# Performance work log

Hardware: AMD Instinct MI355X
Metric: run time of the kernel (lower is better)

The kernel has to match this reference:

```python
import jax, jax.numpy as jnp
import numpy as np

K = 512
U = 2
TEMP_BERN = 0.67
TEMP_CAT = 0.67
EULER = 0.5772156649015329
EPS = 1e-8
UEPS = 1e-6


def setup_inputs() -> dict:
    key = jax.random.key(0)
    ks = jax.random.split(key, 3)
    B, D = 16384, 1024
    inputs = jax.random.normal(ks[0], (B, D), jnp.float32)
    # glorot-normal-ish init for mW
    mW = jax.random.normal(ks[1], (D, K * U), jnp.float32) * jnp.sqrt(2.0 / (D + K * U))
    sW = jnp.full((D, K * U), -5.0, jnp.float32)
    conc1 = jnp.full((K,), 2.0, jnp.float32)
    conc0 = jnp.full((K,), 0.5453, jnp.float32)
    t_pi = jax.random.uniform(ks[2], (D, K), jnp.float32, 4.0, 5.0)
    biases = jnp.full((K * U,), 0.1, jnp.float32)
    return {"inputs": inputs, "mW": mW, "sW": sW, "conc1": conc1,
            "conc0": conc0, "t_pi": t_pi, "biases": biases}


def _uniform(k, shape):
    return jax.random.uniform(k, shape, jnp.float32, UEPS, 1.0 - UEPS)


def reference(inputs, mW, sW, conc1, conc0, t_pi, biases):
    rk = jax.random.split(jax.random.key(42), 4)

    # --- reparameterized weights W = mW + eps * softplus(sW) ---
    sW_sp = jax.nn.softplus(sW)
    eps = jax.lax.stop_gradient(jax.random.normal(rk[0], mW.shape, jnp.float32))
    W = mW + eps * sW_sp
    kl_weights = -0.5 * jnp.mean(2.0 * sW_sp - jnp.square(mW) - jnp.square(sW_sp) + 1.0)
    layer_loss = kl_weights / 60000.0

    # --- IBP: relaxed Bernoulli sample of t_pi ([D, K]) ---
    u = _uniform(rk[1], t_pi.shape)
    logistic = jnp.log(u) - jnp.log1p(-u)
    z_sample = jax.nn.sigmoid((t_pi + logistic) / TEMP_BERN)  # bin_concrete_sample
    z = jnp.tile(z_sample, (1, U))  # [D, K*U], column order u*K+k (as in TF code)

    # Kumaraswamy stick-breaking prior: cumprod along axis 0 (TF default)
    a_sp = jax.nn.softplus(conc1)  # [K]
    b_sp = jax.nn.softplus(conc0)  # [K]
    uk = _uniform(rk[2], t_pi.shape)
    q_u = jnp.power(1.0 - jnp.power(uk, 1.0 / b_sp), 1.0 / a_sp)  # kumaraswamy_sample
    prior_pi = jnp.cumprod(q_u, axis=0)
    q = jax.nn.sigmoid(t_pi)
    kl_z = jnp.sum(q * (jnp.log(q + EPS) - jnp.log(prior_pi + EPS)))

    # KL(Kumaraswamy(a,b) || Beta(1,1)); (beta-1) series term vanishes
    kl_sticks = jnp.sum(((a_sp - 1.0) / a_sp) * (-EULER - jax.scipy.special.digamma(b_sp) - 1.0 / b_sp)
                        + jnp.log(a_sp * b_sp + EPS) - (b_sp - 1.0) / b_sp)
    layer_loss = layer_loss + kl_sticks + kl_z

    W = z * W
    out = inputs @ W + biases  # [B, K*U]

    # --- LWTA activation via Gumbel-softmax over U competitors ---
    logits = out.reshape(-1, K, U)  # [B, K, U]
    g = -jnp.log(-jnp.log(_uniform(rk[3], logits.shape)))
    xi = jax.nn.softmax((logits + g) / TEMP_CAT, axis=-1)  # concrete_sample
    out_act = (logits * xi).reshape(out.shape)
    q_xi = jax.nn.softmax(logits, axis=-1)
    kl_xi = jnp.mean(jnp.sum(q_xi * (jnp.log(q_xi + EPS) - jnp.log(1.0 / U)), axis=1))
    layer_loss = layer_loss + kl_xi

    return out_act, layer_loss
```

## Files before the change

### kernel.cpp

```cpp
#include <hip/hip_runtime.h>
#include <stdint.h>
#include <math.h>

#define B_N   16384
#define D_N   1024
#define K_N   512
#define KU_N  1024
#define EPS_F 1e-8f
#define TEMP  0.67f
#define EULERC 0.5772156649015329f

#define HEPS  524288
#define HU    262144
#define HG    8388608

typedef uint32_t u32;
typedef __attribute__((ext_vector_type(4))) float f32x4;
typedef __attribute__((ext_vector_type(4))) unsigned int u32x4;
typedef __attribute__((ext_vector_type(8))) __bf16 bf16x8;

#define TF_ROT(x, r) (((x) << (r)) | ((x) >> (32 - (r))))

__host__ __device__ static inline void threefry2x32(u32 k0, u32 k1,
                                                    u32 x0, u32 x1,
                                                    u32* o0, u32* o1) {
  u32 ks2 = k0 ^ k1 ^ 0x1BD11BDAu;
  x0 += k0; x1 += k1;
  x0 += x1; x1 = TF_ROT(x1, 13); x1 ^= x0;
  x0 += x1; x1 = TF_ROT(x1, 15); x1 ^= x0;
  x0 += x1; x1 = TF_ROT(x1, 26); x1 ^= x0;
  x0 += x1; x1 = TF_ROT(x1, 6);  x1 ^= x0;
  x0 += k1; x1 += ks2 + 1u;
  x0 += x1; x1 = TF_ROT(x1, 17); x1 ^= x0;
  x0 += x1; x1 = TF_ROT(x1, 29); x1 ^= x0;
  x0 += x1; x1 = TF_ROT(x1, 16); x1 ^= x0;
  x0 += x1; x1 = TF_ROT(x1, 24); x1 ^= x0;
  x0 += ks2; x1 += k0 + 2u;
  x0 += x1; x1 = TF_ROT(x1, 13); x1 ^= x0;
  x0 += x1; x1 = TF_ROT(x1, 15); x1 ^= x0;
  x0 += x1; x1 = TF_ROT(x1, 26); x1 ^= x0;
  x0 += x1; x1 = TF_ROT(x1, 6);  x1 ^= x0;
  x0 += k0; x1 += k1 + 3u;
  x0 += x1; x1 = TF_ROT(x1, 17); x1 ^= x0;
  x0 += x1; x1 = TF_ROT(x1, 29); x1 ^= x0;
  x0 += x1; x1 = TF_ROT(x1, 16); x1 ^= x0;
  x0 += x1; x1 = TF_ROT(x1, 24); x1 ^= x0;
  x0 += k1; x1 += ks2 + 4u;
  x0 += x1; x1 = TF_ROT(x1, 13); x1 ^= x0;
  x0 += x1; x1 = TF_ROT(x1, 15); x1 ^= x0;
  x0 += x1; x1 = TF_ROT(x1, 26); x1 ^= x0;
  x0 += x1; x1 = TF_ROT(x1, 6);  x1 ^= x0;
  x0 += ks2; x1 += k0 + 5u;
  *o0 = x0; *o1 = x1;
}

__device__ static inline float bits_to_u01(u32 b) {
  u32 f = (b >> 9) | 0x3f800000u;
  return __uint_as_float(f) - 1.0f;
}
__device__ static inline float unif_f(u32 b, float lo, float hi) {
  float f = bits_to_u01(b);
  return fmaxf(lo, f * (hi - lo) + lo);
}
__device__ static inline float erfinv_f(float x) {
  float w = -log1pf(-x * x);
  float p;
  if (w < 5.f) {
    w -= 2.5f;
    p = 2.81022636e-08f;
    p = fmaf(p, w, 3.43273939e-07f);
    p = fmaf(p, w, -3.5233877e-06f);
    p = fmaf(p, w, -4.39150654e-06f);
    p = fmaf(p, w, 0.00021858087f);
    p = fmaf(p, w, -0.00125372503f);
    p = fmaf(p, w, -0.00417768164f);
    p = fmaf(p, w, 0.246640727f);
    p = fmaf(p, w, 1.50140941f);
  } else {
    w = sqrtf(w) - 3.f;
    p = -0.000200214257f;
    p = fmaf(p, w, 0.000100950558f);
    p = fmaf(p, w, 0.00134934322f);
    p = fmaf(p, w, -0.00367342844f);
    p = fmaf(p, w, 0.00573950773f);
    p = fmaf(p, w, -0.0076224613f);
    p = fmaf(p, w, 0.00943887047f);
    p = fmaf(p, w, 1.00167406f);
    p = fmaf(p, w, 2.83297682f);
  }
  return p * x;
}
__device__ static inline float softplus_f(float x) {
  return fmaxf(x, 0.f) + log1pf(expf(-fabsf(x)));
}
__device__ static inline float rcp_f(float x) { return __builtin_amdgcn_rcpf(x); }
__device__ static inline float sigmoid_fast(float x) {
  return rcp_f(1.f + __expf(-x));
}
__device__ static inline float digamma_f(float x) {
  float r = 0.f;
  while (x < 6.f) { r -= 1.f / x; x += 1.f; }
  float inv = 1.f / x, inv2 = inv * inv;
  return r + logf(x) - 0.5f * inv
       - inv2 * (1.f / 12.f - inv2 * (1.f / 120.f - inv2 * (1.f / 252.f)));
}
__device__ static inline unsigned short f2bf_rne(float x) {
  u32 u = __float_as_uint(x);
  u32 r = (u + 0x7fffu + ((u >> 16) & 1u)) >> 16;
  return (unsigned short)r;
}
__device__ static inline u32 cvt_pk_bf16(float lo, float hi) {
  u32 r;
  asm("v_cvt_pk_bf16_f32 %0, %1, %2" : "=v"(r) : "v"(lo), "v"(hi));
  return r;
}
__device__ static inline void gload_lds16(const void* g, void* l) {
  __builtin_amdgcn_global_load_lds(
      (const __attribute__((address_space(1))) u32*)g,
      (__attribute__((address_space(3))) u32*)l, 16, 0, 0);
}

__device__ static inline float block_sum(float v) {
  __shared__ float sm[16];
  int lane = threadIdx.x & 63;
  int wid = threadIdx.x >> 6;
  #pragma unroll
  for (int o = 32; o > 0; o >>= 1) v += __shfl_down(v, o, 64);
  if (lane == 0) sm[wid] = v;
  __syncthreads();
  float s = 0.f;
  if (threadIdx.x == 0) {
    int nw = (blockDim.x + 63) >> 6;
    s = sm[0];
    for (int w = 1; w < nw; ++w) s += sm[w];
  }
  return s;
}

__global__ void k_init(const float* __restrict__ conc1,
                       const float* __restrict__ conc0,
                       float* __restrict__ invA, float* __restrict__ invB,
                       float* gacc) {
  int k = threadIdx.x;
  float a = softplus_f(conc1[k]);
  float b = softplus_f(conc0[k]);
  invA[k] = 1.f / a;
  invB[k] = 1.f / b;
  float s = ((a - 1.f) / a) * (-EULERC - digamma_f(b) - 1.f / b)
          + logf(a * b + EPS_F) - (b - 1.f) / b;
  float t = block_sum(s);
  if (threadIdx.x == 0) { gacc[0] = 0.f; gacc[1] = t; gacc[2] = 0.f; }
}

__global__ __launch_bounds__(256) void k_klz_a(const float* __restrict__ invA,
                                               const float* __restrict__ invB,
                                               float* __restrict__ P,
                                               u32 qk0, u32 qk1) {
  int idx = blockIdx.x * 256 + threadIdx.x;
  int c = idx >> 9, k = idx & (K_N - 1);
  float iA = invA[k], iB = invB[k];
  float p = 1.f;
  int d0 = c << 4;
  for (int d = d0; d < d0 + 16; ++d) {
    int n = (d << 9) + k;
    u32 x0 = (n < HU) ? (u32)n : (u32)(n - HU);
    u32 o0, o1;
    threefry2x32(qk0, qk1, x0, x0 + HU, &o0, &o1);
    u32 bits = (n < HU) ? o0 : o1;
    float u = unif_f(bits, 1e-6f, 1.f - 1e-6f);
    p *= powf(1.f - powf(u, iB), iA);
  }
  P[idx] = p;
}

__global__ __launch_bounds__(256) void k_klz_b(const float* __restrict__ t_pi,
                                               const float* __restrict__ invA,
                                               const float* __restrict__ invB,
                                               const float* __restrict__ P,
                                               float* gacc,
                                               u32 qk0, u32 qk1) {
  int idx = blockIdx.x * 256 + threadIdx.x;
  int c = idx >> 9, k = idx & (K_N - 1);
  float iA = invA[k], iB = invB[k];
  float prior = 1.f;
  for (int c2 = 0; c2 < c; ++c2) prior *= P[(c2 << 9) + k];
  float s = 0.f;
  int d0 = c << 4;
  for (int d = d0; d < d0 + 16; ++d) {
    int n = (d << 9) + k;
    u32 x0 = (n < HU) ? (u32)n : (u32)(n - HU);
    u32 o0, o1;
    threefry2x32(qk0, qk1, x0, x0 + HU, &o0, &o1);
    u32 bits = (n < HU) ? o0 : o1;
    float u = unif_f(bits, 1e-6f, 1.f - 1e-6f);
    prior *= powf(1.f - powf(u, iB), iA);
    float q = sigmoid_fast(t_pi[n]);
    s += q * (__logf(q + EPS_F) - __logf(prior + EPS_F));
  }
  float t = block_sum(s);
  if (threadIdx.x == 0) atomicAdd(&gacc[1], t);
}

__global__ __launch_bounds__(256) void k_wbuildT(const float* __restrict__ mW,
                                                 const float* __restrict__ sW,
                                                 const float* __restrict__ t_pi,
                                                 unsigned short* __restrict__ WzT,
                                                 float* __restrict__ gacc,
                                                 u32 ek0, u32 ek1,
                                                 u32 uk0, u32 uk1) {
  __shared__ unsigned short tile[64][65];
  int dt = (int)blockIdx.x >> 4;
  int jt = (int)blockIdx.x & 15;
  int d0 = dt << 6, j0 = jt << 6;
  int tj = threadIdx.x & 63;
  int tr = threadIdx.x >> 6;
  int j = j0 + tj;
  int kk = j & (K_N - 1);
  bool lowD = (dt < 8);
  float klw = 0.f;
  #pragma unroll 4
  for (int rr = 0; rr < 16; ++rr) {
    int dl = (rr << 2) + tr;
    int d = d0 + dl;
    int n = (d << 10) + j;
    u32 x0 = lowD ? (u32)n : (u32)(n - HEPS);
    u32 o0, o1;
    threefry2x32(ek0, ek1, x0, x0 + HEPS, &o0, &o1);
    u32 ebits = lowD ? o0 : o1;
    int nz = (d << 9) + kk;
    u32 zx0 = lowD ? (u32)nz : (u32)(nz - HU);
    u32 z0, z1;
    threefry2x32(uk0, uk1, zx0, zx0 + HU, &z0, &z1);
    u32 zbits = lowD ? z0 : z1;
    float u = unif_f(zbits, 1e-6f, 1.f - 1e-6f);
    float logistic = __logf(u) - log1pf(-u);
    float z = sigmoid_fast((t_pi[nz] + logistic) * (1.f / TEMP));
    float un = unif_f(ebits, -0.99999994f, 1.0f);
    float epsn = 1.41421356f * erfinv_f(un);
    float m = mW[n], sp = softplus_f(sW[n]);
    tile[tj][dl] = f2bf_rne(z * (m + epsn * sp));
    klw += 2.f * sp - m * m - sp * sp + 1.f;
  }
  __syncthreads();
  #pragma unroll 4
  for (int rr = 0; rr < 16; ++rr) {
    int jl = (rr << 2) + tr;
    WzT[(size_t)(j0 + jl) * D_N + d0 + tj] = tile[jl][tj];
  }
  float t = block_sum(klw);
  if (threadIdx.x == 0) atomicAdd(&gacc[0], t);
}

#define GBM 128
#define GBN 128
#define GBK 32

__global__ __launch_bounds__(256) void k_gemm(const float* __restrict__ A,
                                              const unsigned short* __restrict__ Bt,
                                              const float* __restrict__ bias,
                                              float* __restrict__ C) {
  __shared__ __align__(16) unsigned short As[GBM * GBK];
  __shared__ __align__(16) unsigned short Bs[GBN * GBK];

  int f = (int)blockIdx.x;
  int wk = (f & 7) * 128 + (f >> 3);
  const int brow = (wk >> 3) * GBM;
  const int bcol = (wk & 7) * GBN;

  const int tid = threadIdx.x;
  const int lane = tid & 63;
  const int w = tid >> 6;

  const int ar = tid >> 1;
  const int ac = (tid & 1) << 4;
  const float* gA = A + (size_t)(brow + ar) * D_N + ac;
  const int c0 = (tid & 1) << 1;
  char* asw0 = (char*)As + (ar << 6) + (((c0    ) ^ (ar & 3)) << 4);
  char* asw1 = (char*)As + (ar << 6) + (((c0 | 1) ^ (ar & 3)) << 4);

  const int brr = tid >> 2;
  const int bco = ((tid & 3) ^ (brr & 3)) << 3;
  const unsigned short* gB = Bt + (size_t)(bcol + brr) * D_N + bco;

  f32x4 acc[4][4];
  #pragma unroll
  for (int m = 0; m < 4; ++m)
    #pragma unroll
    for (int n = 0; n < 4; ++n) acc[m][n] = (f32x4){0.f, 0.f, 0.f, 0.f};

  const int wr = (w >> 1) << 6;
  const int wc = (w & 1) << 6;
  const int fr = lane & 15;
  const int kg = lane >> 4;

  f32x4 a0 = *(const f32x4*)(gA + 0);
  f32x4 a1 = *(const f32x4*)(gA + 4);
  f32x4 a2 = *(const f32x4*)(gA + 8);
  f32x4 a3 = *(const f32x4*)(gA + 12);

  for (int kt = 0; kt < D_N; kt += GBK) {
    u32x4 p0, p1;
    p0.x = cvt_pk_bf16(a0.x, a0.y); p0.y = cvt_pk_bf16(a0.z, a0.w);
    p0.z = cvt_pk_bf16(a1.x, a1.y); p0.w = cvt_pk_bf16(a1.z, a1.w);
    p1.x = cvt_pk_bf16(a2.x, a2.y); p1.y = cvt_pk_bf16(a2.z, a2.w);
    p1.z = cvt_pk_bf16(a3.x, a3.y); p1.w = cvt_pk_bf16(a3.z, a3.w);
    __syncthreads();
    gload_lds16(gB + kt,            (char*)Bs + (w << 10));
    gload_lds16(gB + 64 * D_N + kt, (char*)Bs + 4096 + (w << 10));
    *(u32x4*)asw0 = p0;
    *(u32x4*)asw1 = p1;
    __syncthreads();
    if (kt + GBK < D_N) {
      const float* g = gA + kt + GBK;
      a0 = *(const f32x4*)(g + 0);
      a1 = *(const f32x4*)(g + 4);
      a2 = *(const f32x4*)(g + 8);
      a3 = *(const f32x4*)(g + 12);
    }
    bf16x8 af[4];
    #pragma unroll
    for (int m = 0; m < 4; ++m) {
      int row = wr + m * 16 + fr;
      af[m] = *(const bf16x8*)((char*)As + (row << 6) + ((kg ^ (row & 3)) << 4));
    }
    #pragma unroll
    for (int n = 0; n < 4; ++n) {
      int col = wc + n * 16 + fr;
      bf16x8 bf = *(const bf16x8*)((char*)Bs + (col << 6) + ((kg ^ (col & 3)) << 4));
      #pragma unroll
      for (int m = 0; m < 4; ++m)
        acc[m][n] = __builtin_amdgcn_mfma_f32_16x16x32_bf16(af[m], bf, acc[m][n], 0, 0, 0);
    }
  }

  #pragma unroll
  for (int n = 0; n < 4; ++n) {
    int col = bcol + wc + n * 16 + fr;
    float bv = bias[col];
    #pragma unroll
    for (int m = 0; m < 4; ++m) {
      int rowb = brow + wr + m * 16 + (kg << 2);
      C[(size_t)(rowb + 0) * KU_N + col] = acc[m][n].x + bv;
      C[(size_t)(rowb + 1) * KU_N + col] = acc[m][n].y + bv;
      C[(size_t)(rowb + 2) * KU_N + col] = acc[m][n].z + bv;
      C[(size_t)(rowb + 3) * KU_N + col] = acc[m][n].w + bv;
    }
  }
}

__device__ static inline float lwta_pair(float v0, float v1, u32 ba, u32 bb,
                                         float* o0, float* o1) {
  float u0 = unif_f(ba, 1e-6f, 1.f - 1e-6f);
  float u1 = unif_f(bb, 1e-6f, 1.f - 1e-6f);
  float g0 = -__logf(-__logf(u0));
  float g1 = -__logf(-__logf(u1));
  const float it = 1.f / TEMP;
  float d = ((v1 + g1) - (v0 + g0)) * it;
  float xi0 = rcp_f(1.f + __expf(d));
  float xi1 = 1.f - xi0;
  *o0 = v0 * xi0;
  *o1 = v1 * xi1;
  float qd = v1 - v0;
  float q0 = rcp_f(1.f + __expf(qd));
  float q1 = 1.f - q0;
  const float LOG2F = 0.6931471805599453f;
  return q0 * (__logf(q0 + EPS_F) + LOG2F) + q1 * (__logf(q1 + EPS_F) + LOG2F);
}

__global__ __launch_bounds__(256) void k_epi(float* __restrict__ C,
                                             float* __restrict__ partial,
                                             u32 gk0, u32 gk1) {
  int idx = blockIdx.x * 256 + threadIdx.x;
  int b = idx >> 9;
  int c2 = (idx & 511) << 1;
  size_t p0 = (size_t)b * KU_N + c2;
  size_t p1 = p0 + (size_t)8192 * KU_N;
  float2 r0 = *(const float2*)&C[p0];
  float2 r1 = *(const float2*)&C[p1];
  u32 m = ((u32)b << 10) | (u32)c2;
  u32 x0a, x1a, x0b, x1b;
  threefry2x32(gk0, gk1, m,      m + HG,      &x0a, &x1a);
  threefry2x32(gk0, gk1, m + 1u, m + 1u + HG, &x0b, &x1b);
  float2 w0, w1;
  float kl = lwta_pair(r0.x, r0.y, x0a, x0b, &w0.x, &w0.y)
           + lwta_pair(r1.x, r1.y, x1a, x1b, &w1.x, &w1.y);
  *(float2*)&C[p0] = w0;
  *(float2*)&C[p1] = w1;
  float t = block_sum(kl);
  if (threadIdx.x == 0) partial[blockIdx.x] = t;
}

#define NPART 16384
__global__ __launch_bounds__(256) void k_final(const float* __restrict__ gacc,
                                               const float* __restrict__ partial,
                                               float* __restrict__ out_loss) {
  float s = 0.f;
  for (int i = threadIdx.x; i < NPART; i += 256) s += partial[i];
  float t = block_sum(s);
  if (threadIdx.x == 0) {
    float kl_weights = -0.5f * (gacc[0] * (1.f / 1048576.f));
    out_loss[0] = kl_weights / 60000.f + gacc[1] + t * (1.f / 32768.f);
  }
}

extern "C" void kernel_launch(void* const* d_in, const int* in_sizes, int n_in,
                              void* d_out, int out_size, void* d_ws, size_t ws_size,
                              hipStream_t stream) {
  (void)in_sizes; (void)n_in; (void)out_size; (void)ws_size;
  const float* inputs = (const float*)d_in[0];
  const float* mW     = (const float*)d_in[1];
  const float* sW     = (const float*)d_in[2];
  const float* conc1  = (const float*)d_in[3];
  const float* conc0  = (const float*)d_in[4];
  const float* t_pi   = (const float*)d_in[5];
  const float* biases = (const float*)d_in[6];
  float* out = (float*)d_out;

  u32 a[4], b[4];
  for (int i = 0; i < 4; ++i)
    threefry2x32(0u, 42u, (u32)i, (u32)(i + 4), &a[i], &b[i]);
  u32 e_k0 = a[0], e_k1 = a[1];
  u32 u_k0 = a[2], u_k1 = a[3];
  u32 q_k0 = b[0], q_k1 = b[1];
  u32 g_k0 = b[2], g_k1 = b[3];

  char* wsb = (char*)d_ws;
  unsigned short* WzT = (unsigned short*)wsb;
  float* P       = (float*)(wsb + (2u << 20));
  float* invA    = (float*)(wsb + (2u << 20) + (128u << 10));
  float* invB    = (float*)(wsb + (2u << 20) + (130u << 10));
  float* gacc    = (float*)(wsb + (2u << 20) + (132u << 10));
  float* partial = (float*)(wsb + (2u << 20) + (136u << 10));

  hipLaunchKernelGGL(k_init, dim3(1), dim3(512), 0, stream,
                     conc1, conc0, invA, invB, gacc);
  hipLaunchKernelGGL(k_klz_a, dim3(128), dim3(256), 0, stream,
                     invA, invB, P, q_k0, q_k1);
  hipLaunchKernelGGL(k_klz_b, dim3(128), dim3(256), 0, stream,
                     t_pi, invA, invB, P, gacc, q_k0, q_k1);
  hipLaunchKernelGGL(k_wbuildT, dim3(256), dim3(256), 0, stream,
                     mW, sW, t_pi, WzT, gacc, e_k0, e_k1, u_k0, u_k1);
  hipLaunchKernelGGL(k_gemm, dim3(1024), dim3(256), 0, stream,
                     inputs, WzT, biases, out);
  hipLaunchKernelGGL(k_epi, dim3(NPART), dim3(256), 0, stream,
                     out, partial, g_k0, g_k1);
  hipLaunchKernelGGL(k_final, dim3(1), dim3(256), 0, stream,
                     gacc, partial, out + 16777216);
}
```

Before: 190.6 us.

## Double-buffer LDS tiles in GEMM to overlap loads with MFMA

The GEMM kernel now keeps two LDS buffers for the A and B tiles. While MFMAs run on the current buffer, the next tile's B global-to-LDS loads and the converted A stores go into the other buffer. This drops one of the two barriers per k-step and aims to hide load latency behind compute. It doubles LDS use to 32KB per block, which may reduce occupancy, and correctness now depends on the async LDS loads completing before the single barrier.

```diff
diff --git a/kernel.cpp b/kernel.cpp
--- a/kernel.cpp
+++ b/kernel.cpp
@@ -259,8 +259,8 @@
                                               const unsigned short* __restrict__ Bt,
                                               const float* __restrict__ bias,
                                               float* __restrict__ C) {
-  __shared__ __align__(16) unsigned short As[GBM * GBK];
-  __shared__ __align__(16) unsigned short Bs[GBN * GBK];
+  __shared__ __align__(16) unsigned short As[2][GBM * GBK];
+  __shared__ __align__(16) unsigned short Bs[2][GBN * GBK];
 
   int f = (int)blockIdx.x;
   int wk = (f & 7) * 128 + (f >> 3);
@@ -275,12 +275,14 @@
   const int ac = (tid & 1) << 4;
   const float* gA = A + (size_t)(brow + ar) * D_N + ac;
   const int c0 = (tid & 1) << 1;
-  char* asw0 = (char*)As + (ar << 6) + (((c0    ) ^ (ar & 3)) << 4);
-  char* asw1 = (char*)As + (ar << 6) + (((c0 | 1) ^ (ar & 3)) << 4);
+  const int aoff0 = (ar << 6) + (((c0    ) ^ (ar & 3)) << 4);
+  const int aoff1 = (ar << 6) + (((c0 | 1) ^ (ar & 3)) << 4);
 
   const int brr = tid >> 2;
   const int bco = ((tid & 3) ^ (brr & 3)) << 3;
   const unsigned short* gB = Bt + (size_t)(bcol + brr) * D_N + bco;
+  const int boff0 = (w << 10);
+  const int boff1 = 4096 + (w << 10);
 
   f32x4 acc[4][4];
   #pragma unroll
@@ -297,40 +299,60 @@
   f32x4 a1 = *(const f32x4*)(gA + 4);
   f32x4 a2 = *(const f32x4*)(gA + 8);
   f32x4 a3 = *(const f32x4*)(gA + 12);
-
-  for (int kt = 0; kt < D_N; kt += GBK) {
+  gload_lds16(gB,            (char*)Bs[0] + boff0);
+  gload_lds16(gB + 64 * D_N, (char*)Bs[0] + boff1);
+  {
     u32x4 p0, p1;
     p0.x = cvt_pk_bf16(a0.x, a0.y); p0.y = cvt_pk_bf16(a0.z, a0.w);
     p0.z = cvt_pk_bf16(a1.x, a1.y); p0.w = cvt_pk_bf16(a1.z, a1.w);
     p1.x = cvt_pk_bf16(a2.x, a2.y); p1.y = cvt_pk_bf16(a2.z, a2.w);
     p1.z = cvt_pk_bf16(a3.x, a3.y); p1.w = cvt_pk_bf16(a3.z, a3.w);
-    __syncthreads();
-    gload_lds16(gB + kt,            (char*)Bs + (w << 10));
-    gload_lds16(gB + 64 * D_N + kt, (char*)Bs + 4096 + (w << 10));
-    *(u32x4*)asw0 = p0;
-    *(u32x4*)asw1 = p1;
-    __syncthreads();
-    if (kt + GBK < D_N) {
-      const float* g = gA + kt + GBK;
-      a0 = *(const f32x4*)(g + 0);
-      a1 = *(const f32x4*)(g + 4);
-      a2 = *(const f32x4*)(g + 8);
-      a3 = *(const f32x4*)(g + 12);
+    *(u32x4*)((char*)As[0] + aoff0) = p0;
+    *(u32x4*)((char*)As[0] + aoff1) = p1;
+  }
+  a0 = *(const f32x4*)(gA + GBK + 0);
+  a1 = *(const f32x4*)(gA + GBK + 4);
+  a2 = *(const f32x4*)(gA + GBK + 8);
+  a3 = *(const f32x4*)(gA + GBK + 12);
+  __syncthreads();
+
+  #pragma unroll 2
+  for (int t = 0; t < 32; ++t) {
+    const int cur = t & 1;
+    if (t < 31) {
+      const int ktn = (t + 1) << 5;
+      gload_lds16(gB + ktn,            (char*)Bs[cur ^ 1] + boff0);
+      gload_lds16(gB + 64 * D_N + ktn, (char*)Bs[cur ^ 1] + boff1);
+      u32x4 p0, p1;
+      p0.x = cvt_pk_bf16(a0.x, a0.y); p0.y = cvt_pk_bf16(a0.z, a0.w);
+      p0.z = cvt_pk_bf16(a1.x, a1.y); p0.w = cvt_pk_bf16(a1.z, a1.w);
+      p1.x = cvt_pk_bf16(a2.x, a2.y); p1.y = cvt_pk_bf16(a2.z, a2.w);
+      p1.z = cvt_pk_bf16(a3.x, a3.y); p1.w = cvt_pk_bf16(a3.z, a3.w);
+      *(u32x4*)((char*)As[cur ^ 1] + aoff0) = p0;
+      *(u32x4*)((char*)As[cur ^ 1] + aoff1) = p1;
+      if (t < 30) {
+        const float* g = gA + ((t + 2) << 5);
+        a0 = *(const f32x4*)(g + 0);
+        a1 = *(const f32x4*)(g + 4);
+        a2 = *(const f32x4*)(g + 8);
+        a3 = *(const f32x4*)(g + 12);
+      }
     }
     bf16x8 af[4];
     #pragma unroll
     for (int m = 0; m < 4; ++m) {
       int row = wr + m * 16 + fr;
-      af[m] = *(const bf16x8*)((char*)As + (row << 6) + ((kg ^ (row & 3)) << 4));
+      af[m] = *(const bf16x8*)((char*)As[cur] + (row << 6) + ((kg ^ (row & 3)) << 4));
     }
     #pragma unroll
     for (int n = 0; n < 4; ++n) {
       int col = wc + n * 16 + fr;
-      bf16x8 bf = *(const bf16x8*)((char*)Bs + (col << 6) + ((kg ^ (col & 3)) << 4));
+      bf16x8 bf = *(const bf16x8*)((char*)Bs[cur] + (col << 6) + ((kg ^ (col & 3)) << 4));
       #pragma unroll
       for (int m = 0; m < 4; ++m)
         acc[m][n] = __builtin_amdgcn_mfma_f32_16x16x32_bf16(af[m], bf, acc[m][n], 0, 0, 0);
     }
+    __syncthreads();
   }
 
   #pragma unroll
```

New measurement: 192.7 us. Within noise of the previous version (+1.1%).
